# Kernel tuning notes

Measured on AMD Instinct MI355X. Metric: run time of the kernel, lower is better.

## Reference

```python
import jax, jax.numpy as jnp
import numpy as np

N_NODES = 100000


def gcn_conv(x, W, b, src, dst, deg_inv_sqrt, n):
    # x: [N, Fin] -> h: [N, Fout]; message = norm * h[src], scatter-add to dst
    h = x @ W
    norm = deg_inv_sqrt[src] * deg_inv_sqrt[dst]  # [E]
    msgs = h[src] * norm[:, None]                 # [E, Fout]
    out = jax.ops.segment_sum(msgs, dst, num_segments=n)
    return out + b


def setup_inputs() -> dict:
    key = jax.random.key(0)
    k_x, k_e, k_w1, k_w2 = jax.random.split(key, 4)
    x = jax.random.normal(k_x, (N_NODES, 3), dtype=jnp.float32)
    edge_index = jax.random.randint(k_e, (2, 3200000), 0, N_NODES, dtype=jnp.int64)
    # Glorot-style init matching PyG GCNConv defaults (weight + bias)
    W1 = jax.random.normal(k_w1, (3, 16), dtype=jnp.float32) * (1.0 / np.sqrt(3))
    b1 = jnp.zeros((16,), dtype=jnp.float32)
    W2 = jax.random.normal(k_w2, (16, 1), dtype=jnp.float32) * (1.0 / np.sqrt(16))
    b2 = jnp.zeros((1,), dtype=jnp.float32)
    return {"x": x, "edge_index": edge_index, "W1": W1, "b1": b1, "W2": W2, "b2": b2}


def reference(x, edge_index, W1, b1, W2, b2):
    n = x.shape[0]
    # add self-loops (PyG GCNConv default add_self_loops=True)
    loops = jnp.arange(n, dtype=edge_index.dtype)
    src = jnp.concatenate([edge_index[0], loops])
    dst = jnp.concatenate([edge_index[1], loops])
    # symmetric normalization D^{-1/2} (A+I) D^{-1/2}
    deg = jax.ops.segment_sum(jnp.ones_like(src, dtype=x.dtype), dst, num_segments=n)
    deg_inv_sqrt = jnp.where(deg > 0, jax.lax.rsqrt(deg), 0.0)
    h = jax.nn.relu(gcn_conv(x, W1, b1, src, dst, deg_inv_sqrt, n))
    out = gcn_conv(h, W2, b2, src, dst, deg_inv_sqrt, n)
    return out
```

## Files before the change

kernel.cpp:

```cpp
#include <hip/hip_runtime.h>


#define NPR 256
#define RNG 391
#define BINB 512
#define TPB_BIN 512
#define LCAP 40
#define KCAP 48
#define CTPB 512
#define GTPB 256
#define NSLOT (BINB * KCAP)
#define NQUAD (NSLOT / 4)
#define QPT (NQUAD / CTPB)
#define SCAP 56
#define NCAP 72
#define CSRSTRIDE (NCAP * NPR)

__global__ __launch_bounds__(TPB_BIN) void k_bin(const int* __restrict__ src,
                                                 const int* __restrict__ dst,
                                                 int E, int n,
                                                 unsigned int* __restrict__ bucket,
                                                 int* __restrict__ bcnt) {
    __shared__ unsigned int staged[RNG * LCAP];
    __shared__ int cur[RNG];
    int b = blockIdx.x;
    for (int r = threadIdx.x; r < RNG; r += TPB_BIN) cur[r] = 0;
    __syncthreads();
    int G = E >> 2;
    int gchunk = (G + BINB - 1) / BINB;
    int g0 = b * gchunk, g1 = min(g0 + gchunk, G);
    const int4* src4 = (const int4*)src;
    const int4* dst4 = (const int4*)dst;
    for (int g = g0 + threadIdx.x; g < g1; g += TPB_BIN) {
        int4 sv = src4[g];
        int4 dv = dst4[g];
        int ss[4] = {sv.x, sv.y, sv.z, sv.w};
        int dd[4] = {dv.x, dv.y, dv.z, dv.w};
#pragma unroll
        for (int k = 0; k < 4; ++k) {
            int s = ss[k], d = dd[k];
            if ((unsigned)s >= (unsigned)n || (unsigned)d >= (unsigned)n) continue;
            int r = d >> 8;
            int dl = d & 255;
            unsigned int ent = ((unsigned)dl << 17) | (unsigned)s;
            int slot = atomicAdd(&cur[r], 1);
            if (slot < LCAP)
                staged[r * LCAP + slot] = ent;
            else if (slot < KCAP)
                bucket[((size_t)r * BINB + b) * KCAP + slot] = ent;
        }
    }
    if (b == BINB - 1) {
        for (int e = (G << 2) + threadIdx.x; e < E; e += TPB_BIN) {
            int s = src[e], d = dst[e];
            if ((unsigned)s >= (unsigned)n || (unsigned)d >= (unsigned)n) continue;
            int r = d >> 8;
            unsigned int ent = ((unsigned)(d & 255) << 17) | (unsigned)s;
            int slot = atomicAdd(&cur[r], 1);
            if (slot < LCAP) staged[r * LCAP + slot] = ent;
            else if (slot < KCAP) bucket[((size_t)r * BINB + b) * KCAP + slot] = ent;
        }
    }
    __syncthreads();
    for (int fi = threadIdx.x; fi < RNG * LCAP; fi += TPB_BIN) {
        int r = fi / LCAP;
        int e = fi - r * LCAP;
        if (e < min(cur[r], LCAP))
            bucket[((size_t)r * BINB + b) * KCAP + e] = staged[fi];
    }
    for (int r = threadIdx.x; r < RNG; r += TPB_BIN)
        bcnt[r * BINB + b] = min(cur[r], KCAP);
}

__global__ __launch_bounds__(CTPB) void k_csr(const int* __restrict__ bcnt,
                                              const unsigned int* __restrict__ bucket,
                                              unsigned int* __restrict__ csr,
                                              const float* __restrict__ x,
                                              float4* __restrict__ gx,
                                              int* __restrict__ degl, int n) {
    __shared__ unsigned int staged[SCAP * NPR];
    __shared__ int cur[NPR];
    __shared__ int cnt_s[BINB];
    int r = blockIdx.x;
    for (int t = threadIdx.x; t < NPR; t += CTPB) cur[t] = 0;
    for (int t = threadIdx.x; t < BINB; t += CTPB) cnt_s[t] = bcnt[r * BINB + t];
    __syncthreads();
    const uint4* base4 = (const uint4*)(bucket + (size_t)r * NSLOT);
    unsigned int* crow = csr + (size_t)r * CSRSTRIDE;
#pragma unroll
    for (int p = 0; p < QPT; ++p) {
        int idx = threadIdx.x + p * CTPB;
        int slot0 = idx << 2;
        int b = slot0 / KCAP;
        int j0 = slot0 - b * KCAP;
        int c = cnt_s[b];
        if (j0 >= c) continue;
        uint4 q = base4[idx];
        unsigned int es[4] = {q.x, q.y, q.z, q.w};
#pragma unroll
        for (int k = 0; k < 4; ++k) {
            if (j0 + k < c) {
                unsigned int ent = es[k];
                int dl = ent >> 17;
                unsigned int s = ent & 0x1FFFFu;
                int slot = atomicAdd(&cur[dl], 1);
                if (slot < SCAP)
                    staged[(slot << 8) | dl] = s;
                else if (slot < NCAP)
                    crow[(slot << 8) | dl] = s;
            }
        }
    }
    __syncthreads();
    for (int idx = threadIdx.x; idx < SCAP * NPR; idx += CTPB) {
        int slot = idx >> 8;
        int dl = idx & 255;
        if (slot < min(cur[dl], SCAP))
            crow[idx] = staged[idx];
    }
    for (int t = threadIdx.x; t < NPR; t += CTPB) {
        int i = (r << 8) + t;
        if (i < n) {
            int dg = cur[t];
            degl[i] = min(dg, NCAP);
            float dv = rsqrtf((float)dg + 1.0f);
            float4 o;
            o.x = dv * x[i * 3 + 0];
            o.y = dv * x[i * 3 + 1];
            o.z = dv * x[i * 3 + 2];
            o.w = dv;
            gx[i] = o;
        }
    }
}

__global__ __launch_bounds__(GTPB) void k_gather1(const unsigned int* __restrict__ csr,
                                                  const int* __restrict__ degl,
                                                  const float4* __restrict__ gx,
                                                  const float* __restrict__ W1,
                                                  const float* __restrict__ b1,
                                                  const float* __restrict__ W2,
                                                  float* __restrict__ g2, int n) {
    int t = blockIdx.x * GTPB + threadIdx.x;
    int i = t >> 2, q = t & 3;
    if (i >= n) return;
    int r = i >> 8;
    int dl = i & 255;
    const unsigned int* lst = csr + (size_t)r * CSRSTRIDE + dl;
    int len = degl[i];
    float sx = 0.f, sy = 0.f, sz = 0.f;
#pragma unroll 2
    for (int j = q; j < len; j += 4) {
        float4 v = gx[lst[(size_t)j << 8]];
        sx += v.x; sy += v.y; sz += v.z;
    }
    sx += __shfl_xor(sx, 1); sy += __shfl_xor(sy, 1); sz += __shfl_xor(sz, 1);
    sx += __shfl_xor(sx, 2); sy += __shfl_xor(sy, 2); sz += __shfl_xor(sz, 2);
    if (q) return;
    float4 me = gx[i];
    sx += me.x; sy += me.y; sz += me.z;
    float dv = me.w;
    float acc = 0.0f;
#pragma unroll
    for (int f = 0; f < 16; ++f) {
        float h = b1[f] + dv * (sx * W1[f] + sy * W1[16 + f] + sz * W1[32 + f]);
        acc += fmaxf(h, 0.0f) * W2[f];
    }
    g2[i] = dv * acc;
}

__global__ __launch_bounds__(GTPB) void k_gather2(const unsigned int* __restrict__ csr,
                                                  const int* __restrict__ degl,
                                                  const float4* __restrict__ gx,
                                                  const float* __restrict__ g2,
                                                  const float* __restrict__ b2,
                                                  float* __restrict__ out, int n) {
    int t = blockIdx.x * GTPB + threadIdx.x;
    int i = t >> 2, q = t & 3;
    if (i >= n) return;
    int r = i >> 8;
    int dl = i & 255;
    const unsigned int* lst = csr + (size_t)r * CSRSTRIDE + dl;
    int len = degl[i];
    float o = 0.f;
#pragma unroll 2
    for (int j = q; j < len; j += 4)
        o += g2[lst[(size_t)j << 8]];
    o += __shfl_xor(o, 1);
    o += __shfl_xor(o, 2);
    if (q) return;
    out[i] = b2[0] + gx[i].w * (g2[i] + o);
}

extern "C" void kernel_launch(void* const* d_in, const int* in_sizes, int n_in,
                              void* d_out, int out_size, void* d_ws, size_t ws_size,
                              hipStream_t stream) {
    const float* x  = (const float*)d_in[0];
    const int*   ei = (const int*)d_in[1];
    const float* W1 = (const float*)d_in[2];
    const float* b1 = (const float*)d_in[3];
    const float* W2 = (const float*)d_in[4];
    const float* b2 = (const float*)d_in[5];
    float* out = (float*)d_out;

    const int n = in_sizes[0] / 3;
    const int E = in_sizes[1] / 2;
    const int* src = ei;
    const int* dst = ei + E;

    char* ws = (char*)d_ws;
    size_t off = 0;
    unsigned int* bucket = (unsigned int*)(ws + off); off += (size_t)RNG * NSLOT * 4;
    unsigned int* csr    = (unsigned int*)(ws + off); off += (size_t)RNG * CSRSTRIDE * 4;
    int*          bcnt   = (int*)(ws + off);          off += (size_t)RNG * BINB * 4;
    float4*       gx     = (float4*)(ws + off);       off += (size_t)n * 16;
    float*        g2     = (float*)(ws + off);        off += (size_t)n * 4;
    int*          degl   = (int*)(ws + off);          off += (size_t)n * 4;

    int blk_g = (4 * n + GTPB - 1) / GTPB;

    k_bin<<<BINB, TPB_BIN, 0, stream>>>(src, dst, E, n, bucket, bcnt);
    k_csr<<<RNG, CTPB, 0, stream>>>(bcnt, bucket, csr, x, gx, degl, n);
    k_gather1<<<blk_g, GTPB, 0, stream>>>(csr, degl, gx, W1, b1, W2, g2, n);
    k_gather2<<<blk_g, GTPB, 0, stream>>>(csr, degl, gx, g2, b2, out, n);
}
```

Before: 141.2 us.

## Store CSR rows contiguously per node and gather with one thread per node

Changes the CSR layout from slot-major interleaved (stride 256) to node-major contiguous rows, so each node's neighbor list can be read as uint4 vectors. The gather kernels now use one thread per node with an unrolled 14-quad loop instead of four threads per node with shuffle reductions. This cuts the number of scattered index loads and removes the cross-lane reductions, but each thread's row reads are strided across lanes (72 words apart) and the thread count drops fourfold, which lowers memory-level parallelism. The k_bin LDS staging capacity shrinks to 32 so it can use shift indexing, which pushes more entries to global memory.

```diff
diff --git a/kernel.cpp b/kernel.cpp
--- a/kernel.cpp
+++ b/kernel.cpp
@@ -5,7 +5,7 @@
 #define RNG 391
 #define BINB 512
 #define TPB_BIN 512
-#define LCAP 40
+#define LCAP 32
 #define KCAP 48
 #define CTPB 512
 #define GTPB 256
@@ -14,7 +14,8 @@
 #define QPT (NQUAD / CTPB)
 #define SCAP 56
 #define NCAP 72
-#define CSRSTRIDE (NCAP * NPR)
+#define CSRSTRIDE (NPR * NCAP)
+#define GQ 14
 
 __global__ __launch_bounds__(TPB_BIN) void k_bin(const int* __restrict__ src,
                                                  const int* __restrict__ dst,
@@ -41,11 +42,10 @@
             int s = ss[k], d = dd[k];
             if ((unsigned)s >= (unsigned)n || (unsigned)d >= (unsigned)n) continue;
             int r = d >> 8;
-            int dl = d & 255;
-            unsigned int ent = ((unsigned)dl << 17) | (unsigned)s;
+            unsigned int ent = ((unsigned)(d & 255) << 17) | (unsigned)s;
             int slot = atomicAdd(&cur[r], 1);
             if (slot < LCAP)
-                staged[r * LCAP + slot] = ent;
+                staged[(r << 5) | slot] = ent;
             else if (slot < KCAP)
                 bucket[((size_t)r * BINB + b) * KCAP + slot] = ent;
         }
@@ -57,14 +57,13 @@
             int r = d >> 8;
             unsigned int ent = ((unsigned)(d & 255) << 17) | (unsigned)s;
             int slot = atomicAdd(&cur[r], 1);
-            if (slot < LCAP) staged[r * LCAP + slot] = ent;
+            if (slot < LCAP) staged[(r << 5) | slot] = ent;
             else if (slot < KCAP) bucket[((size_t)r * BINB + b) * KCAP + slot] = ent;
         }
     }
     __syncthreads();
     for (int fi = threadIdx.x; fi < RNG * LCAP; fi += TPB_BIN) {
-        int r = fi / LCAP;
-        int e = fi - r * LCAP;
+        int r = fi >> 5, e = fi & 31;
         if (e < min(cur[r], LCAP))
             bucket[((size_t)r * BINB + b) * KCAP + e] = staged[fi];
     }
@@ -78,7 +77,7 @@
                                               const float* __restrict__ x,
                                               float4* __restrict__ gx,
                                               int* __restrict__ degl, int n) {
-    __shared__ unsigned int staged[SCAP * NPR];
+    __shared__ unsigned int staged[NPR * SCAP];
     __shared__ int cur[NPR];
     __shared__ int cnt_s[BINB];
     int r = blockIdx.x;
@@ -90,9 +89,8 @@
 #pragma unroll
     for (int p = 0; p < QPT; ++p) {
         int idx = threadIdx.x + p * CTPB;
-        int slot0 = idx << 2;
-        int b = slot0 / KCAP;
-        int j0 = slot0 - b * KCAP;
+        int b = idx / 12;
+        int j0 = (idx - b * 12) << 2;
         int c = cnt_s[b];
         if (j0 >= c) continue;
         uint4 q = base4[idx];
@@ -105,18 +103,18 @@
                 unsigned int s = ent & 0x1FFFFu;
                 int slot = atomicAdd(&cur[dl], 1);
                 if (slot < SCAP)
-                    staged[(slot << 8) | dl] = s;
+                    staged[dl * SCAP + slot] = s;
                 else if (slot < NCAP)
-                    crow[(slot << 8) | dl] = s;
+                    crow[dl * NCAP + slot] = s;
             }
         }
     }
     __syncthreads();
-    for (int idx = threadIdx.x; idx < SCAP * NPR; idx += CTPB) {
-        int slot = idx >> 8;
-        int dl = idx & 255;
+    for (int idx = threadIdx.x; idx < NPR * NCAP; idx += CTPB) {
+        int dl = idx / NCAP;
+        int slot = idx - dl * NCAP;
         if (slot < min(cur[dl], SCAP))
-            crow[idx] = staged[idx];
+            crow[idx] = staged[dl * SCAP + slot];
     }
     for (int t = threadIdx.x; t < NPR; t += CTPB) {
         int i = (r << 8) + t;
@@ -141,25 +139,31 @@
                                                   const float* __restrict__ b1,
                                                   const float* __restrict__ W2,
                                                   float* __restrict__ g2, int n) {
-    int t = blockIdx.x * GTPB + threadIdx.x;
-    int i = t >> 2, q = t & 3;
+    int i = blockIdx.x * GTPB + threadIdx.x;
     if (i >= n) return;
-    int r = i >> 8;
-    int dl = i & 255;
-    const unsigned int* lst = csr + (size_t)r * CSRSTRIDE + dl;
+    int r = i >> 8, dl = i & 255;
+    const uint4* row4 = (const uint4*)(csr + (size_t)r * CSRSTRIDE + dl * NCAP);
     int len = degl[i];
-    float sx = 0.f, sy = 0.f, sz = 0.f;
-#pragma unroll 2
-    for (int j = q; j < len; j += 4) {
-        float4 v = gx[lst[(size_t)j << 8]];
-        sx += v.x; sy += v.y; sz += v.z;
-    }
-    sx += __shfl_xor(sx, 1); sy += __shfl_xor(sy, 1); sz += __shfl_xor(sz, 1);
-    sx += __shfl_xor(sx, 2); sy += __shfl_xor(sy, 2); sz += __shfl_xor(sz, 2);
-    if (q) return;
     float4 me = gx[i];
-    sx += me.x; sy += me.y; sz += me.z;
-    float dv = me.w;
+    float sx = me.x, sy = me.y, sz = me.z, dv = me.w;
+#pragma unroll
+    for (int q = 0; q < GQ; ++q) {
+        int base = q << 2;
+        if (base < len) {
+            uint4 v = row4[q];
+            int rem = len - base;
+            float4 a = gx[v.x]; sx += a.x; sy += a.y; sz += a.z;
+            if (rem > 1) { float4 b = gx[v.y]; sx += b.x; sy += b.y; sz += b.z; }
+            if (rem > 2) { float4 c = gx[v.z]; sx += c.x; sy += c.y; sz += c.z; }
+            if (rem > 3) { float4 e = gx[v.w]; sx += e.x; sy += e.y; sz += e.z; }
+        }
+    }
+    if (len > GQ * 4) {
+        const unsigned int* row = (const unsigned int*)row4;
+        for (int j = GQ * 4; j < len; ++j) {
+            float4 a = gx[row[j]]; sx += a.x; sy += a.y; sz += a.z;
+        }
+    }
     float acc = 0.0f;
 #pragma unroll
     for (int f = 0; f < 16; ++f) {
@@ -175,21 +179,29 @@
                                                   const float* __restrict__ g2,
                                                   const float* __restrict__ b2,
                                                   float* __restrict__ out, int n) {
-    int t = blockIdx.x * GTPB + threadIdx.x;
-    int i = t >> 2, q = t & 3;
+    int i = blockIdx.x * GTPB + threadIdx.x;
     if (i >= n) return;
-    int r = i >> 8;
-    int dl = i & 255;
-    const unsigned int* lst = csr + (size_t)r * CSRSTRIDE + dl;
+    int r = i >> 8, dl = i & 255;
+    const uint4* row4 = (const uint4*)(csr + (size_t)r * CSRSTRIDE + dl * NCAP);
     int len = degl[i];
-    float o = 0.f;
-#pragma unroll 2
-    for (int j = q; j < len; j += 4)
-        o += g2[lst[(size_t)j << 8]];
-    o += __shfl_xor(o, 1);
-    o += __shfl_xor(o, 2);
-    if (q) return;
-    out[i] = b2[0] + gx[i].w * (g2[i] + o);
+    float o = g2[i];
+#pragma unroll
+    for (int q = 0; q < GQ; ++q) {
+        int base = q << 2;
+        if (base < len) {
+            uint4 v = row4[q];
+            int rem = len - base;
+            o += g2[v.x];
+            if (rem > 1) o += g2[v.y];
+            if (rem > 2) o += g2[v.z];
+            if (rem > 3) o += g2[v.w];
+        }
+    }
+    if (len > GQ * 4) {
+        const unsigned int* row = (const unsigned int*)row4;
+        for (int j = GQ * 4; j < len; ++j) o += g2[row[j]];
+    }
+    out[i] = b2[0] + gx[i].w * o;
 }
 
 extern "C" void kernel_launch(void* const* d_in, const int* in_sizes, int n_in,
@@ -217,7 +229,7 @@
     float*        g2     = (float*)(ws + off);        off += (size_t)n * 4;
     int*          degl   = (int*)(ws + off);          off += (size_t)n * 4;
 
-    int blk_g = (4 * n + GTPB - 1) / GTPB;
+    int blk_g = (n + GTPB - 1) / GTPB;
 
     k_bin<<<BINB, TPB_BIN, 0, stream>>>(src, dst, E, n, bucket, bcnt);
     k_csr<<<RNG, CTPB, 0, stream>>>(bcnt, bucket, csr, x, gx, degl, n);
```

New measurement: 158.4 us. 12.2% more time.
